# Kernel optimization log

Measured on AMD Instinct MI355X. Metric: run time of the kernel, lower is better.

Reference implementation:

```python
import jax, jax.numpy as jnp
import numpy as np

N_X_AXIS = 128
N_Y_AXIS = 128
X_RANGE = (-2.0, 2.0)
Y_RANGE = (-2.0, 2.0)
L_SCALE = 1.0


def _make_grid():
    # grid[k*n_x + j] = (x_j, y_k), y counted BACKWARDS (top row = max y)
    xs = jnp.linspace(X_RANGE[0], X_RANGE[1], N_X_AXIS, dtype=jnp.float32)
    ys = jnp.linspace(Y_RANGE[1], Y_RANGE[0], N_Y_AXIS, dtype=jnp.float32)
    gx, gy = jnp.meshgrid(xs, ys)  # (n_y, n_x) each
    return jnp.stack([gx, gy], axis=-1).reshape(-1, 2)  # (G, 2)


def setup_inputs() -> dict:
    key = jax.random.key(0)
    k1, k2 = jax.random.split(key)
    X = jax.random.normal(k1, (8192, 2), dtype=jnp.float32)
    Y = jax.random.normal(k2, (8192, 2), dtype=jnp.float32)
    return {"X": X, "Y": Y}


def reference(X, Y):
    grid = _make_grid()  # (G, 2), constant buffer
    l_scale = jnp.exp(jnp.clip(jnp.log(jnp.float32(L_SCALE)), -5.0, 5.0))
    # RBF Gram matrix between grid points and context points: (G, n)
    d2 = jnp.sum((grid[:, None, :] - X[None, :, :]) ** 2, axis=-1)
    Gram = jnp.exp(-0.5 * d2 / (l_scale ** 2))
    # Psi: prepend a ones column -> (n, 3)
    Expand_Y = jnp.concatenate([jnp.ones((Y.shape[0], 1), dtype=Y.dtype), Y], axis=1)
    Feature_Map = Gram @ Expand_Y  # (G, 3): channel 0 = density
    # normalize smoothing channels by density channel
    norm_fm = jnp.concatenate(
        [Feature_Map[:, :1], Feature_Map[:, 1:] / Feature_Map[:, :1]], axis=1
    )
    # (G,3) -> (n_y, n_x, 3) -> (1, 3, n_y, n_x)
    return jnp.transpose(norm_fm.reshape(N_Y_AXIS, N_X_AXIS, 3), (2, 0, 1))[None]
```

## Files before the change

### kernel.cpp

```cpp
#include <hip/hip_runtime.h>

#define G_TOTAL 16384
#define NPTS    8192
#define CI      128
#define NSPLIT  64
#define LDA     136
#define PBLK    12288

typedef _Float16 f16;
typedef f16  f16x8 __attribute__((ext_vector_type(8)));
typedef f16  f16x4 __attribute__((ext_vector_type(4)));
typedef float f32x4 __attribute__((ext_vector_type(4)));

__device__ __forceinline__ float fast_exp2(float x) {
#if __has_builtin(__builtin_amdgcn_exp2f)
    return __builtin_amdgcn_exp2f(x);
#else
    float r; asm("v_exp_f32 %0, %1" : "=v"(r) : "v"(x)); return r;
#endif
}

__global__ __launch_bounds__(256) void enc_mfma(
    const float* __restrict__ X,
    const float* __restrict__ Y,
    f16* __restrict__ wsP)
{
    __shared__ f16 ExT[128 * LDA];
    __shared__ f16 Ey3[3 * 32 * LDA];

    const int t    = threadIdx.x;
    const int b    = blockIdx.x;
    const int tile = b & 3;
    const int sidx = b >> 2;
    const int c0   = sidx * CI;
    const int kb   = tile * 32;

    const float sc   = 0.84932184f;
    const float step = 4.0f / 127.0f;

    const float2* X2 = (const float2*)X;
    const float2* Y2 = (const float2*)Y;

    {
        const int   j  = t >> 1, ih = (t & 1) * 64;
        const float gx = (-2.0f + step * (float)j) * sc;
#pragma unroll
        for (int u = 0; u < 8; ++u) {
            f16x8 v;
#pragma unroll
            for (int e = 0; e < 8; ++e) {
                const int   i = ih + u * 8 + e;
                const float d = gx - X2[c0 + i].x * sc;
                v[e] = (f16)fast_exp2(-d * d);
            }
            *(f16x8*)&ExT[j * LDA + ih + u * 8] = v;
        }
    }
    {
        const int   k  = t >> 3, ib = (t & 7) * 16;
        const float gy = (2.0f - step * (float)(kb + k)) * sc;
#pragma unroll
        for (int u = 0; u < 2; ++u) {
            f16x8 v0, v1, v2;
#pragma unroll
            for (int e = 0; e < 8; ++e) {
                const int    i  = ib + u * 8 + e;
                const float  d  = gy - X2[c0 + i].y * sc;
                const float  ee = fast_exp2(-d * d);
                const float2 yv = Y2[c0 + i];
                v0[e] = (f16)ee;
                v1[e] = (f16)(ee * yv.x);
                v2[e] = (f16)(ee * yv.y);
            }
            *(f16x8*)&Ey3[(0 * 32 + k) * LDA + ib + u * 8] = v0;
            *(f16x8*)&Ey3[(1 * 32 + k) * LDA + ib + u * 8] = v1;
            *(f16x8*)&Ey3[(2 * 32 + k) * LDA + ib + u * 8] = v2;
        }
    }
    __syncthreads();

    const int w    = t >> 6;
    const int lane = t & 63;
    const int l15  = lane & 15;
    const int lk8  = (lane >> 4) * 8;

    f32x4 acc[12];
#pragma unroll
    for (int z = 0; z < 12; ++z) acc[z] = (f32x4){0.f, 0.f, 0.f, 0.f};

#pragma unroll
    for (int ks = 0; ks < 4; ++ks) {
        const int io = ks * 32 + lk8;
        const f16x8 bf0 = *(const f16x8*)&ExT[(w * 32 +      l15) * LDA + io];
        const f16x8 bf1 = *(const f16x8*)&ExT[(w * 32 + 16 + l15) * LDA + io];
#pragma unroll
        for (int c = 0; c < 3; ++c) {
            const f16x8 a0 = *(const f16x8*)&Ey3[(c * 32 +      l15) * LDA + io];
            const f16x8 a1 = *(const f16x8*)&Ey3[(c * 32 + 16 + l15) * LDA + io];
            acc[c*4+0] = __builtin_amdgcn_mfma_f32_16x16x32_f16(a0, bf0, acc[c*4+0], 0, 0, 0);
            acc[c*4+1] = __builtin_amdgcn_mfma_f32_16x16x32_f16(a0, bf1, acc[c*4+1], 0, 0, 0);
            acc[c*4+2] = __builtin_amdgcn_mfma_f32_16x16x32_f16(a1, bf0, acc[c*4+2], 0, 0, 0);
            acc[c*4+3] = __builtin_amdgcn_mfma_f32_16x16x32_f16(a1, bf1, acc[c*4+3], 0, 0, 0);
        }
    }

    f16* P = wsP + (size_t)(tile * NSPLIT + sidx) * PBLK;
#pragma unroll
    for (int f = 0; f < 12; ++f) {
        f16x4 pv;
        pv[0] = (f16)acc[f][0];  pv[1] = (f16)acc[f][1];
        pv[2] = (f16)acc[f][2];  pv[3] = (f16)acc[f][3];
        *(f16x4*)&P[((w * 12 + f) * 64 + lane) * 4] = pv;
    }
}

__global__ __launch_bounds__(512) void reduce_norm(
    const f16* __restrict__ wsP, float* __restrict__ out)
{
    __shared__ f32x4 sm[8][3][64];

    const int bx   = blockIdx.x;
    const int tile = bx >> 4;
    const int w    = (bx >> 2) & 3;
    const int q    = bx & 3;
    const int t    = threadIdx.x;
    const int lane = t & 63;
    const int sq   = t >> 6;

    const f16x4* base = (const f16x4*)wsP;
    const int slot = (w * 12 + q) * 64 + lane;

    f32x4 s0 = {0.f,0.f,0.f,0.f}, s1 = s0, s2 = s0;
#pragma unroll 8
    for (int s = sq * 8; s < sq * 8 + 8; ++s) {
        const size_t bo = (size_t)(tile * NSPLIT + s) * 3072 + slot;
        const f16x4 h0 = base[bo];
        const f16x4 h1 = base[bo + 256];
        const f16x4 h2 = base[bo + 512];
#pragma unroll
        for (int r = 0; r < 4; ++r) {
            s0[r] += (float)h0[r];
            s1[r] += (float)h1[r];
            s2[r] += (float)h2[r];
        }
    }
    sm[sq][0][lane] = s0;
    sm[sq][1][lane] = s1;
    sm[sq][2][lane] = s2;
    __syncthreads();

    if (t < 64) {
        f32x4 f0 = {0.f,0.f,0.f,0.f}, f1 = f0, f2 = f0;
#pragma unroll
        for (int u = 0; u < 8; ++u) {
#pragma unroll
            for (int r = 0; r < 4; ++r) {
                f0[r] += sm[u][0][t][r];
                f1[r] += sm[u][1][t][r];
                f2[r] += sm[u][2][t][r];
            }
        }
        const int k0 = tile * 32 + (q >> 1) * 16 + (t >> 4) * 4;
        const int j  = w * 32 + (q & 1) * 16 + (t & 15);
#pragma unroll
        for (int r = 0; r < 4; ++r) {
            const int   g   = (k0 + r) * 128 + j;
            const float inv = 1.0f / f0[r];
            out[g]               = f0[r];
            out[G_TOTAL + g]     = f1[r] * inv;
            out[2 * G_TOTAL + g] = f2[r] * inv;
        }
    }
}

extern "C" void kernel_launch(void* const* d_in, const int* in_sizes, int n_in,
                              void* d_out, int out_size, void* d_ws, size_t ws_size,
                              hipStream_t stream) {
    const float* X = (const float*)d_in[0];
    const float* Y = (const float*)d_in[1];
    float* out = (float*)d_out;
    f16*  wsP = (f16*)d_ws;

    enc_mfma<<<256, 256, 0, stream>>>(X, Y, wsP);
    reduce_norm<<<64, 512, 0, stream>>>(wsP, out);
}
```

Measured before the change: 64.21 us.

## Fuse encode and reduction into one cooperative kernel with grid sync

Merges the MFMA encode kernel and the partial-sum reduction kernel into a single cooperative launch separated by a grid-wide barrier, and spreads the reduction across all 256 blocks instead of 64. The goal is to remove the second kernel launch and its launch gap, and to use more parallelism for the reduction. In exchange it adds the cost of a grid sync and the requirement that all 256 blocks be co-resident, and each block's reduction step has less work.

```diff
diff --git a/kernel.cpp b/kernel.cpp
--- a/kernel.cpp
+++ b/kernel.cpp
@@ -1,4 +1,7 @@
 #include <hip/hip_runtime.h>
+#include <hip/hip_cooperative_groups.h>
+
+namespace cg = cooperative_groups;
 
 #define G_TOTAL 16384
 #define NPTS    8192
@@ -20,10 +23,11 @@
 #endif
 }
 
-__global__ __launch_bounds__(256) void enc_mfma(
+__global__ __launch_bounds__(256) void enc_reduce_coop(
     const float* __restrict__ X,
     const float* __restrict__ Y,
-    f16* __restrict__ wsP)
+    f16* __restrict__ wsP,
+    float* __restrict__ out)
 {
     __shared__ f16 ExT[128 * LDA];
     __shared__ f16 Ey3[3 * 32 * LDA];
@@ -112,31 +116,30 @@
         pv[2] = (f16)acc[f][2];  pv[3] = (f16)acc[f][3];
         *(f16x4*)&P[((w * 12 + f) * 64 + lane) * 4] = pv;
     }
-}
 
-__global__ __launch_bounds__(512) void reduce_norm(
-    const f16* __restrict__ wsP, float* __restrict__ out)
-{
-    __shared__ f32x4 sm[8][3][64];
+    cg::this_grid().sync();
 
-    const int bx   = blockIdx.x;
-    const int tile = bx >> 4;
-    const int w    = (bx >> 2) & 3;
-    const int q    = bx & 3;
-    const int t    = threadIdx.x;
-    const int lane = t & 63;
-    const int sq   = t >> 6;
+    f32x4* sm = (f32x4*)ExT;
 
-    const f16x4* base = (const f16x4*)wsP;
-    const int slot = (w * 12 + q) * 64 + lane;
+    const int bx    = blockIdx.x;
+    const int tile2 = bx >> 6;
+    const int w2    = (bx >> 4) & 3;
+    const int q2    = (bx >> 2) & 3;
+    const int lh    = bx & 3;
+    const int l16   = t & 15;
+    const int sq    = t >> 4;
+    const int lane2 = lh * 16 + l16;
+
+    const f16x4* basep = (const f16x4*)wsP;
+    const int slot = (w2 * 12 + q2) * 64 + lane2;
 
     f32x4 s0 = {0.f,0.f,0.f,0.f}, s1 = s0, s2 = s0;
-#pragma unroll 8
-    for (int s = sq * 8; s < sq * 8 + 8; ++s) {
-        const size_t bo = (size_t)(tile * NSPLIT + s) * 3072 + slot;
-        const f16x4 h0 = base[bo];
-        const f16x4 h1 = base[bo + 256];
-        const f16x4 h2 = base[bo + 512];
+#pragma unroll
+    for (int s = sq * 4; s < sq * 4 + 4; ++s) {
+        const size_t bo = (size_t)(tile2 * NSPLIT + s) * 3072 + slot;
+        const f16x4 h0 = basep[bo];
+        const f16x4 h1 = basep[bo + 256];
+        const f16x4 h2 = basep[bo + 512];
 #pragma unroll
         for (int r = 0; r < 4; ++r) {
             s0[r] += (float)h0[r];
@@ -144,24 +147,24 @@
             s2[r] += (float)h2[r];
         }
     }
-    sm[sq][0][lane] = s0;
-    sm[sq][1][lane] = s1;
-    sm[sq][2][lane] = s2;
+    sm[(sq * 3 + 0) * 16 + l16] = s0;
+    sm[(sq * 3 + 1) * 16 + l16] = s1;
+    sm[(sq * 3 + 2) * 16 + l16] = s2;
     __syncthreads();
 
-    if (t < 64) {
+    if (t < 16) {
         f32x4 f0 = {0.f,0.f,0.f,0.f}, f1 = f0, f2 = f0;
 #pragma unroll
-        for (int u = 0; u < 8; ++u) {
+        for (int u = 0; u < 16; ++u) {
 #pragma unroll
             for (int r = 0; r < 4; ++r) {
-                f0[r] += sm[u][0][t][r];
-                f1[r] += sm[u][1][t][r];
-                f2[r] += sm[u][2][t][r];
+                f0[r] += sm[(u * 3 + 0) * 16 + t][r];
+                f1[r] += sm[(u * 3 + 1) * 16 + t][r];
+                f2[r] += sm[(u * 3 + 2) * 16 + t][r];
             }
         }
-        const int k0 = tile * 32 + (q >> 1) * 16 + (t >> 4) * 4;
-        const int j  = w * 32 + (q & 1) * 16 + (t & 15);
+        const int k0 = tile2 * 32 + (q2 >> 1) * 16 + lh * 4;
+        const int j  = w2 * 32 + (q2 & 1) * 16 + t;
 #pragma unroll
         for (int r = 0; r < 4; ++r) {
             const int   g   = (k0 + r) * 128 + j;
@@ -181,6 +184,7 @@
     float* out = (float*)d_out;
     f16*  wsP = (f16*)d_ws;
 
-    enc_mfma<<<256, 256, 0, stream>>>(X, Y, wsP);
-    reduce_norm<<<64, 512, 0, stream>>>(wsP, out);
+    void* args[] = {(void*)&X, (void*)&Y, (void*)&wsP, (void*)&out};
+    hipLaunchCooperativeKernel((void*)enc_reduce_coop,
+                               dim3(256), dim3(256), args, 0, stream);
 }
```

After: 105.4 us. 64.2% more time.
